# Performance work log

Measured on AMD Instinct MI355X. Metric: run time of the kernel, lower is better.

Reference implementation:

```python
import jax, jax.numpy as jnp
import numpy as np

EPS = 1e-5  # torch LayerNorm default eps
ALIBI_SLOPE = 1.0

def layer_norm(x, g, b):
    mu = x.mean(-1, keepdims=True)
    var = ((x - mu) ** 2).mean(-1, keepdims=True)
    return (x - mu) * jax.lax.rsqrt(var + EPS) * g + b

def setup_inputs() -> dict:
    key = jax.random.key(0)
    B, T, D, DK, F = 4, 4096, 1024, 128, 2048  # F = ffn_mult * d_model
    ks = jax.random.split(key, 6)
    def s(k, shp, fan):
        return jax.random.normal(k, shp, jnp.float32) / np.sqrt(fan).astype(np.float32)
    return {
        'x': jax.random.normal(ks[0], (B, T, D), jnp.float32),
        'ln1_g': jnp.ones((D,), jnp.float32), 'ln1_b': jnp.zeros((D,), jnp.float32),
        'Wq': s(ks[1], (DK, D), D),  # torch Linear weight layout (out, in)
        'Wk': s(ks[2], (DK, D), D),
        'Wv': s(ks[3], (D, D), D),
        'ln2_g': jnp.ones((D,), jnp.float32), 'ln2_b': jnp.zeros((D,), jnp.float32),
        'W1': s(ks[4], (F, D), D), 'b1': jnp.zeros((F,), jnp.float32),
        'W2': s(ks[5], (D, F), F), 'b2': jnp.zeros((D,), jnp.float32),
    }

def reference(x, ln1_g, ln1_b, Wq, Wk, Wv, ln2_g, ln2_b, W1, b1, W2, b2):
    B, T, D = x.shape
    dk = Wq.shape[0]
    h = layer_norm(x, ln1_g, ln1_b)
    q = jnp.einsum('btd,kd->btk', h, Wq)
    k = jnp.einsum('btd,kd->btk', h, Wk)
    att = jnp.einsum('btk,bsk->bts', q, k) * (dk ** -0.5)  # [B,T,T]
    pos = jnp.arange(T)
    dist = jnp.clip(pos[:, None] - pos[None, :], 0).astype(att.dtype)
    att = att - ALIBI_SLOPE * dist  # alibi bias
    causal = pos[:, None] >= pos[None, :]
    att = jnp.where(causal, att, -jnp.inf)
    att = jax.nn.softmax(att, axis=-1)
    ctx = jnp.einsum('bts,bsd->btd', att, h)  # note: attends over h, not a v-projection
    x = x + jnp.einsum('btd,ed->bte', ctx, Wv)
    h2 = layer_norm(x, ln2_g, ln2_b)
    ff = jnp.maximum(jnp.einsum('btd,fd->btf', h2, W1) + b1, 0.0)
    x = x + jnp.einsum('btf,df->btd', ff, W2) + b2
    return x
```

## Files before the change

kernel.cpp:

```cpp
#include <hip/hip_runtime.h>
#include <stdint.h>

typedef __attribute__((ext_vector_type(4))) float f32x4;
typedef __attribute__((ext_vector_type(8))) unsigned short u16x8;
typedef __attribute__((ext_vector_type(4))) unsigned short u16x4;
typedef unsigned short bf16_t;

#define DEV __device__ __forceinline__

DEV void mfma16(f32x4& d, u16x8 a, u16x8 b) {
    asm("v_mfma_f32_16x16x32_bf16 %0, %1, %2, %0" : "+v"(d) : "v"(a), "v"(b));
}

DEV bf16_t f2bf(float f) {
    uint32_t u = __builtin_bit_cast(uint32_t, f);
    return (bf16_t)((u + 0x7fffu + ((u >> 16) & 1u)) >> 16);
}

DEV void async_g2l16(const void* g, void* l) {
    __builtin_amdgcn_global_load_lds(
        (const __attribute__((address_space(1))) uint32_t*)(uintptr_t)g,
        (__attribute__((address_space(3))) uint32_t*)(uint32_t)(uintptr_t)l,
        16, 0, 0);
}

DEV void blockbar() {
    asm volatile("" ::: "memory");
    __builtin_amdgcn_s_barrier();
    asm volatile("" ::: "memory");
}

#define VMCNT(n) asm volatile("s_waitcnt vmcnt(" #n ")" ::: "memory")

#define MFMA_QUAD(M0, AF, BF)                                                                              \
    __builtin_amdgcn_s_setprio(1);                                                                         \
    mfma16(acc[M0+0][0],AF[0],BF[0]); mfma16(acc[M0+0][1],AF[0],BF[1]); mfma16(acc[M0+0][2],AF[0],BF[2]); mfma16(acc[M0+0][3],AF[0],BF[3]); \
    mfma16(acc[M0+1][0],AF[1],BF[0]); mfma16(acc[M0+1][1],AF[1],BF[1]); mfma16(acc[M0+1][2],AF[1],BF[2]); mfma16(acc[M0+1][3],AF[1],BF[3]); \
    mfma16(acc[M0+2][0],AF[2],BF[0]); mfma16(acc[M0+2][1],AF[2],BF[1]); mfma16(acc[M0+2][2],AF[2],BF[2]); mfma16(acc[M0+2][3],AF[2],BF[3]); \
    mfma16(acc[M0+3][0],AF[3],BF[0]); mfma16(acc[M0+3][1],AF[3],BF[1]); mfma16(acc[M0+3][2],AF[3],BF[2]); mfma16(acc[M0+3][3],AF[3],BF[3]); \
    __builtin_amdgcn_s_setprio(0)

template <int EPI>
__global__ __launch_bounds__(512, 2) void gemm256_nt(
    const bf16_t* __restrict__ A, const bf16_t* __restrict__ B,
    void* __restrict__ Cp, const float* __restrict__ bias,
    const float* __restrict__ res, int M, int N, int K)
{
    __shared__ bf16_t sA[4 * 8192];
    __shared__ bf16_t sB[4 * 8192];
    const int tid = threadIdx.x;
    const int wave = tid >> 6, lane = tid & 63;
    const int lcol = lane & 15, krow = lane >> 4;
    const int wm = wave >> 2, wn = wave & 3;

    int id  = blockIdx.y * gridDim.x + blockIdx.x;
    int nwg = gridDim.x * gridDim.y;
    int swz = ((nwg & 7) == 0) ? ((id & 7) * (nwg >> 3) + (id >> 3)) : id;
    const int bn = swz % gridDim.y;
    const int bm = swz / gridDim.y;
    const int row_a = bm * 256, col_c = bn * 256;

    const int tq = tid >> 2;
    const int tr = (((tid & 3) ^ ((tid >> 3) & 3)) * 8);
    const bf16_t* aSt = A + (size_t)(row_a + tq) * K + tr;
    const bf16_t* bSt = B + (size_t)(col_c + tq) * K + tr;
    const size_t rowstep = (size_t)128 * K;
    bf16_t* ldsAw = sA + wave * 512;
    bf16_t* ldsBw = sB + wave * 512;

    const int cswz = (krow ^ ((lcol >> 1) & 3)) * 8;
    const int raOff = (wm * 128 + lcol) * 32 + cswz;
    const int rbOff = (wn * 64  + lcol) * 32 + cswz;

    f32x4 acc[8][4] = {};
    const int nt = K >> 6;

    async_g2l16(aSt,                ldsAw);
    async_g2l16(aSt + rowstep,      ldsAw + 4096);
    async_g2l16(bSt,                ldsBw);
    async_g2l16(bSt + rowstep,      ldsBw + 4096);
    async_g2l16(aSt + 32,           ldsAw + 8192);
    async_g2l16(aSt + 32 + rowstep, ldsAw + 8192 + 4096);
    async_g2l16(bSt + 32,           ldsBw + 8192);
    async_g2l16(bSt + 32 + rowstep, ldsBw + 8192 + 4096);
    VMCNT(4);
    blockbar();

    for (int t = 0; t < nt; ++t) {
        const int rbase = (t & 1) ? 16384 : 0;
        const int wbase = (t & 1) ? 0 : 16384;
        const bool pf = (t + 1) < nt;
        const size_t ko = (size_t)(t + 1) * 64;
        u16x8 fa[4], fb[4];

#pragma unroll
        for (int i = 0; i < 4; i++) fa[i] = *(const u16x8*)&sA[rbase + raOff + i * 512];
#pragma unroll
        for (int i = 0; i < 4; i++) fb[i] = *(const u16x8*)&sB[rbase + rbOff + i * 512];
        if (pf) { async_g2l16(aSt + ko,           ldsAw + wbase);
                  async_g2l16(aSt + ko + rowstep, ldsAw + wbase + 4096); }
        blockbar();
        MFMA_QUAD(0, fa, fb);
        blockbar();

#pragma unroll
        for (int i = 0; i < 4; i++) fa[i] = *(const u16x8*)&sA[rbase + raOff + 2048 + i * 512];
        if (pf) { async_g2l16(bSt + ko,           ldsBw + wbase);
                  async_g2l16(bSt + ko + rowstep, ldsBw + wbase + 4096); }
        blockbar();
        MFMA_QUAD(4, fa, fb);
        if (pf) { VMCNT(4); } else { VMCNT(0); }
        blockbar();

#pragma unroll
        for (int i = 0; i < 4; i++) fa[i] = *(const u16x8*)&sA[rbase + 8192 + raOff + i * 512];
#pragma unroll
        for (int i = 0; i < 4; i++) fb[i] = *(const u16x8*)&sB[rbase + 8192 + rbOff + i * 512];
        if (pf) { async_g2l16(aSt + ko + 32,           ldsAw + wbase + 8192);
                  async_g2l16(aSt + ko + 32 + rowstep, ldsAw + wbase + 8192 + 4096); }
        blockbar();
        MFMA_QUAD(0, fa, fb);
        blockbar();

#pragma unroll
        for (int i = 0; i < 4; i++) fa[i] = *(const u16x8*)&sA[rbase + 8192 + raOff + 2048 + i * 512];
        if (pf) { async_g2l16(bSt + ko + 32,           ldsBw + wbase + 8192);
                  async_g2l16(bSt + ko + 32 + rowstep, ldsBw + wbase + 8192 + 4096); }
        blockbar();
        MFMA_QUAD(4, fa, fb);
        if (pf) { VMCNT(4); }
        blockbar();
    }

#pragma unroll
    for (int mi = 0; mi < 8; mi++)
#pragma unroll
        for (int ni = 0; ni < 4; ni++)
#pragma unroll
            for (int j = 0; j < 4; j++) {
                const int gr = row_a + wm * 128 + mi * 16 + krow * 4 + j;
                const int gc = col_c + wn * 64 + ni * 16 + lcol;
                float v = acc[mi][ni][j];
                if (EPI == 0) {
                    ((bf16_t*)Cp)[(size_t)gr * N + gc] = f2bf(v);
                } else if (EPI == 1) {
                    v += bias[gc];
                    v = fmaxf(v, 0.f);
                    ((bf16_t*)Cp)[(size_t)gr * N + gc] = f2bf(v);
                } else if (EPI == 2) {
                    ((float*)Cp)[(size_t)gr * N + gc] = v + res[(size_t)gr * N + gc];
                } else {
                    ((float*)Cp)[(size_t)gr * N + gc] = v + bias[gc] + res[(size_t)gr * N + gc];
                }
            }
}

template <int EPI>
__global__ __launch_bounds__(256) void gemm_nt(
    const bf16_t* __restrict__ A, const bf16_t* __restrict__ B,
    void* __restrict__ Cp, const float* __restrict__ bias,
    const float* __restrict__ res, int M, int N, int K)
{
    alignas(16) __shared__ bf16_t sA[128 * 32];
    alignas(16) __shared__ bf16_t sB[128 * 32];
    const int tid = threadIdx.x;
    const int wave = tid >> 6, lane = tid & 63;
    const int lcol = lane & 15, krow = lane >> 4;

    int id  = blockIdx.y * gridDim.x + blockIdx.x;
    int nwg = gridDim.x * gridDim.y;
    int swz = ((nwg & 7) == 0) ? ((id & 7) * (nwg >> 3) + (id >> 3)) : id;
    const int bn = swz % gridDim.y;
    const int bm = swz / gridDim.y;

    const int row_a = bm * 128, col_c = bn * 128;
    const int wm = (wave >> 1) * 64, wn = (wave & 1) * 64;

    const int   srow  = wave * 16 + (lane >> 2);
    const int   scol  = (lane & 3) * 8;
    const bf16_t* aSrc = A + (size_t)(row_a + srow) * K + scol;
    const bf16_t* bSrc = B + (size_t)(col_c + srow) * K + scol;
    char* sAl = (char*)sA + wave * 1024;
    char* sBl = (char*)sB + wave * 1024;
    const size_t rstep = (size_t)64 * K;

    f32x4 acc[4][4] = {};

    for (int k0 = 0; k0 < K; k0 += 32) {
        async_g2l16(aSrc + k0,         sAl);
        async_g2l16(aSrc + k0 + rstep, sAl + 4096);
        async_g2l16(bSrc + k0,         sBl);
        async_g2l16(bSrc + k0 + rstep, sBl + 4096);
        __syncthreads();
        u16x8 af[4], bfr[4];
#pragma unroll
        for (int i = 0; i < 4; i++) {
            af[i]  = *(const u16x8*)&sA[(wm + i * 16 + lcol) * 32 + krow * 8];
            bfr[i] = *(const u16x8*)&sB[(wn + i * 16 + lcol) * 32 + krow * 8];
        }
#pragma unroll
        for (int mi = 0; mi < 4; mi++)
#pragma unroll
            for (int ni = 0; ni < 4; ni++)
                mfma16(acc[mi][ni], af[mi], bfr[ni]);
        __syncthreads();
    }

#pragma unroll
    for (int mi = 0; mi < 4; mi++)
#pragma unroll
        for (int ni = 0; ni < 4; ni++)
#pragma unroll
            for (int j = 0; j < 4; j++) {
                const int gr = row_a + wm + mi * 16 + krow * 4 + j;
                const int gc = col_c + wn + ni * 16 + lcol;
                float v = acc[mi][ni][j];
                if (EPI == 0) {
                    ((bf16_t*)Cp)[(size_t)gr * N + gc] = f2bf(v);
                } else if (EPI == 1) {
                    v += bias[gc];
                    v = fmaxf(v, 0.f);
                    ((bf16_t*)Cp)[(size_t)gr * N + gc] = f2bf(v);
                } else if (EPI == 2) {
                    ((float*)Cp)[(size_t)gr * N + gc] = v + res[(size_t)gr * N + gc];
                } else {
                    ((float*)Cp)[(size_t)gr * N + gc] = v + bias[gc] + res[(size_t)gr * N + gc];
                }
            }
}

__global__ __launch_bounds__(256) void ln_kernel(
    const float* __restrict__ X, const float* __restrict__ G,
    const float* __restrict__ Bt, bf16_t* __restrict__ O)
{
    const int row = blockIdx.x, tid = threadIdx.x;
    const int wave = tid >> 6, lane = tid & 63;
    const size_t base = (size_t)row * 1024 + tid * 4;
    f32x4 xv = *(const f32x4*)&X[base];
    float s  = xv[0] + xv[1] + xv[2] + xv[3];
    float s2 = xv[0]*xv[0] + xv[1]*xv[1] + xv[2]*xv[2] + xv[3]*xv[3];
#pragma unroll
    for (int o = 1; o < 64; o <<= 1) { s += __shfl_xor(s, o); s2 += __shfl_xor(s2, o); }
    __shared__ float red[8];
    if (lane == 0) { red[wave] = s; red[wave + 4] = s2; }
    __syncthreads();
    s  = red[0] + red[1] + red[2] + red[3];
    s2 = red[4] + red[5] + red[6] + red[7];
    const float mu = s * (1.f / 1024.f);
    const float rs = rsqrtf(s2 * (1.f / 1024.f) - mu * mu + 1e-5f);
    f32x4 gv = *(const f32x4*)&G[tid * 4];
    f32x4 bv = *(const f32x4*)&Bt[tid * 4];
    u16x4 ov;
#pragma unroll
    for (int i = 0; i < 4; i++) ov[i] = f2bf((xv[i] - mu) * rs * gv[i] + bv[i]);
    *(u16x4*)&O[base] = ov;
}

__global__ __launch_bounds__(256) void cvt_f32_bf16(
    const float* __restrict__ src, bf16_t* __restrict__ dst, int n)
{
    int i = (blockIdx.x * 256 + threadIdx.x) * 4;
    if (i >= n) return;
    f32x4 v = *(const f32x4*)&src[i];
    u16x4 o;
#pragma unroll
    for (int t = 0; t < 4; t++) o[t] = f2bf(v[t]);
    *(u16x4*)&dst[i] = o;
}

__global__ __launch_bounds__(256) void attn_p(
    const bf16_t* __restrict__ QK, bf16_t* __restrict__ P, int T)
{
    const int tid = threadIdx.x, w = tid >> 6, lane = tid & 63;
    const int lcol = lane & 15, krow = lane >> 4;
    const int qt = blockIdx.x;
    const int ntb = T >> 6;
    const int b = qt / ntb;
    const int r0 = (qt - b * ntb) << 6;
    const size_t g0 = (size_t)b * T + r0;
    const int jbase = r0 - 192;
    const float scale = 0.08838834764831845f;

    __shared__ float lred[2][4][64];

    u16x8 qf[4][4];
#pragma unroll
    for (int mf = 0; mf < 4; mf++)
#pragma unroll
        for (int ks = 0; ks < 4; ks++)
            qf[mf][ks] = *(const u16x8*)&QK[(g0 + mf * 16 + lcol) * 256 + ks * 32 + krow * 8];

    f32x4 acc[4][4] = {};
    const size_t kbase = (size_t)b * T * 256 + 128;
#pragma unroll
    for (int ks = 0; ks < 4; ks++) {
        u16x8 kf[4];
#pragma unroll
        for (int nf = 0; nf < 4; nf++) {
            int jc = jbase + w * 64 + nf * 16 + lcol;
            int jr = jc < 0 ? 0 : jc;
            kf[nf] = *(const u16x8*)&QK[kbase + (size_t)jr * 256 + ks * 32 + krow * 8];
        }
#pragma unroll
        for (int mf = 0; mf < 4; mf++)
#pragma unroll
            for (int nf = 0; nf < 4; nf++)
                mfma16(acc[mf][nf], qf[mf][ks], kf[nf]);
    }

#pragma unroll
    for (int mf = 0; mf < 4; mf++)
#pragma unroll
        for (int j = 0; j < 4; j++) {
            const int i_ = r0 + mf * 16 + krow * 4 + j;
            float m = -1e30f;
#pragma unroll
            for (int nf = 0; nf < 4; nf++) {
                const int jc = jbase + w * 64 + nf * 16 + lcol;
                float sv = (jc >= 0 && jc <= i_) ? acc[mf][nf][j] * scale - (float)(i_ - jc) : -1e30f;
                acc[mf][nf][j] = sv;
                m = fmaxf(m, sv);
            }
#pragma unroll
            for (int o = 1; o < 16; o <<= 1) m = fmaxf(m, __shfl_xor(m, o));
            if (lcol == 0) lred[0][w][mf * 16 + krow * 4 + j] = m;
        }
    __syncthreads();

#pragma unroll
    for (int mf = 0; mf < 4; mf++)
#pragma unroll
        for (int j = 0; j < 4; j++) {
            const int rr = mf * 16 + krow * 4 + j;
            const float m = fmaxf(fmaxf(lred[0][0][rr], lred[0][1][rr]),
                                  fmaxf(lred[0][2][rr], lred[0][3][rr]));
            float sm = 0.f;
#pragma unroll
            for (int nf = 0; nf < 4; nf++) {
                float p = __expf(acc[mf][nf][j] - m);
                acc[mf][nf][j] = p;
                sm += p;
            }
#pragma unroll
            for (int o = 1; o < 16; o <<= 1) sm += __shfl_xor(sm, o);
            if (lcol == 0) lred[1][w][rr] = sm;
        }
    __syncthreads();

    float inv_l[4][4];
#pragma unroll
    for (int mf = 0; mf < 4; mf++)
#pragma unroll
        for (int j = 0; j < 4; j++) {
            const int rr = mf * 16 + krow * 4 + j;
            inv_l[mf][j] = 1.f / (lred[1][0][rr] + lred[1][1][rr] + lred[1][2][rr] + lred[1][3][rr]);
        }
#pragma unroll
    for (int mf = 0; mf < 4; mf++)
#pragma unroll
        for (int nf = 0; nf < 4; nf++)
#pragma unroll
            for (int j = 0; j < 4; j++) {
                const int rr = mf * 16 + krow * 4 + j;
                P[((size_t)qt * 64 + rr) * 256 + w * 64 + nf * 16 + lcol] =
                    f2bf(acc[mf][nf][j] * inv_l[mf][j]);
            }
}

__global__ __launch_bounds__(256) void pv_gemm(
    const bf16_t* __restrict__ P, const bf16_t* __restrict__ H,
    bf16_t* __restrict__ CTX, int T)
{
    alignas(16) __shared__ bf16_t sHt[128 * 40];
    const int tid = threadIdx.x, w = tid >> 6, lane = tid & 63;
    const int lcol = lane & 15, krow = lane >> 4;
    const int qt = blockIdx.x, d0 = blockIdx.y * 128;
    const int ntb = T >> 6, b = qt / ntb;
    const int r0 = (qt - b * ntb) << 6;
    const int jbase = r0 - 192;
    const int wm = (w >> 1) * 32, wn = (w & 1) * 64;
    const int kk = tid >> 3, seg = tid & 7;

    f32x4 acc[2][4] = {};
    for (int k0 = 0; k0 < 256; k0 += 32) {
        int j = jbase + k0 + kk;
        if (j < 0) j = 0;
        const bf16_t* hp = H + ((size_t)b * T + j) * 1024 + d0 + seg * 16;
        u16x8 v0 = *(const u16x8*)hp;
        u16x8 v1 = *(const u16x8*)(hp + 8);
        __syncthreads();
#pragma unroll
        for (int i = 0; i < 8; i++) {
            sHt[(seg * 16 + i) * 40 + kk]     = v0[i];
            sHt[(seg * 16 + 8 + i) * 40 + kk] = v1[i];
        }
        __syncthreads();
        u16x8 af[2], bfr[4];
#pragma unroll
        for (int mi = 0; mi < 2; mi++)
            af[mi] = *(const u16x8*)&P[((size_t)qt * 64 + wm + mi * 16 + lcol) * 256 + k0 + krow * 8];
#pragma unroll
        for (int ni = 0; ni < 4; ni++)
            bfr[ni] = *(const u16x8*)&sHt[(wn + ni * 16 + lcol) * 40 + krow * 8];
#pragma unroll
        for (int mi = 0; mi < 2; mi++)
#pragma unroll
            for (int ni = 0; ni < 4; ni++)
                mfma16(acc[mi][ni], af[mi], bfr[ni]);
    }
#pragma unroll
    for (int mi = 0; mi < 2; mi++)
#pragma unroll
        for (int ni = 0; ni < 4; ni++)
#pragma unroll
            for (int j = 0; j < 4; j++)
                CTX[((size_t)b * T + r0 + wm + mi * 16 + krow * 4 + j) * 1024 +
                    d0 + wn + ni * 16 + lcol] = f2bf(acc[mi][ni][j]);
}

extern "C" void kernel_launch(void* const* d_in, const int* in_sizes, int n_in,
                              void* d_out, int out_size, void* d_ws, size_t ws_size,
                              hipStream_t stream)
{
    const float* x   = (const float*)d_in[0];
    const float* g1  = (const float*)d_in[1];
    const float* be1 = (const float*)d_in[2];
    const float* Wq  = (const float*)d_in[3];
    const float* Wk  = (const float*)d_in[4];
    const float* Wv  = (const float*)d_in[5];
    const float* g2  = (const float*)d_in[6];
    const float* be2 = (const float*)d_in[7];
    const float* W1  = (const float*)d_in[8];
    const float* b1  = (const float*)d_in[9];
    const float* W2  = (const float*)d_in[10];
    const float* b2  = (const float*)d_in[11];

    const int B = 4, T = 4096, D = 1024, DK = 128, F = 2048;
    const int BT = B * T;

    char* ws = (char*)d_ws;
    size_t off = 0;
    auto alloc = [&](size_t bytes) {
        void* p = ws + off;
        off += (bytes + 255) & ~(size_t)255;
        return p;
    };
    bf16_t* wqk_b = (bf16_t*)alloc((size_t)2 * DK * D * 2);
    bf16_t* wv_b  = (bf16_t*)alloc((size_t)D * D * 2);
    bf16_t* w1_b  = (bf16_t*)alloc((size_t)F * D * 2);
    bf16_t* w2_b  = (bf16_t*)alloc((size_t)D * F * 2);
    bf16_t* h     = (bf16_t*)alloc((size_t)BT * D * 2);
    bf16_t* qk    = (bf16_t*)alloc((size_t)BT * 256 * 2);
    bf16_t* P     = (bf16_t*)alloc((size_t)BT * 256 * 2);
    bf16_t* ctx   = (bf16_t*)alloc((size_t)BT * D * 2);
    bf16_t* ff    = (bf16_t*)alloc((size_t)BT * F * 2);
    if (ws_size < off) return;
    float* x2 = (float*)d_out;

    cvt_f32_bf16<<<DK * D / 1024, 256, 0, stream>>>(Wq, wqk_b, DK * D);
    cvt_f32_bf16<<<DK * D / 1024, 256, 0, stream>>>(Wk, wqk_b + (size_t)DK * D, DK * D);
    cvt_f32_bf16<<<D * D / 1024, 256, 0, stream>>>(Wv, wv_b, D * D);
    cvt_f32_bf16<<<F * D / 1024, 256, 0, stream>>>(W1, w1_b, F * D);
    cvt_f32_bf16<<<D * F / 1024, 256, 0, stream>>>(W2, w2_b, D * F);

    ln_kernel<<<BT, 256, 0, stream>>>(x, g1, be1, h);

    gemm_nt<0><<<dim3(BT / 128, 2), 256, 0, stream>>>(h, wqk_b, qk, nullptr, nullptr, BT, 256, D);

    attn_p<<<BT / 64, 256, 0, stream>>>(qk, P, T);
    pv_gemm<<<dim3(BT / 64, D / 128), 256, 0, stream>>>(P, h, ctx, T);

    gemm256_nt<2><<<dim3(BT / 256, D / 256), 512, 0, stream>>>(ctx, wv_b, x2, nullptr, x, BT, D, D);

    ln_kernel<<<BT, 256, 0, stream>>>(x2, g2, be2, h);

    gemm256_nt<1><<<dim3(BT / 256, F / 256), 512, 0, stream>>>(h, w1_b, ff, b1, nullptr, BT, F, D);

    gemm256_nt<3><<<dim3(BT / 256, D / 256), 512, 0, stream>>>(ff, w2_b, x2, b2, x2, BT, D, F);
}
```

Measured before the change: 346.7 us.

## Shrink GEMM tile to 256x128 with K-step 32 and simpler double buffer

Replaces the 256x256 GEMM with a 256x128 tile that uses a 32-wide K step, a single-stage double buffer and one barrier per iteration. It also raises the occupancy hint from 2 to 4 blocks. Halving LDS and accumulator registers per block is meant to give more resident blocks and more tiles across the CUs for these mid-sized GEMMs. In exchange, each loaded byte is reused less, the wait and barrier run every 32 K, and the finer interleave of loads and MFMAs is lost.

Result: slower. 360.4 us (+4.0%).

```diff
diff --git a/kernel.cpp b/kernel.cpp
--- a/kernel.cpp
+++ b/kernel.cpp
@@ -32,33 +32,25 @@
 
 #define VMCNT(n) asm volatile("s_waitcnt vmcnt(" #n ")" ::: "memory")
 
-#define MFMA_QUAD(M0, AF, BF)                                                                              \
-    __builtin_amdgcn_s_setprio(1);                                                                         \
-    mfma16(acc[M0+0][0],AF[0],BF[0]); mfma16(acc[M0+0][1],AF[0],BF[1]); mfma16(acc[M0+0][2],AF[0],BF[2]); mfma16(acc[M0+0][3],AF[0],BF[3]); \
-    mfma16(acc[M0+1][0],AF[1],BF[0]); mfma16(acc[M0+1][1],AF[1],BF[1]); mfma16(acc[M0+1][2],AF[1],BF[2]); mfma16(acc[M0+1][3],AF[1],BF[3]); \
-    mfma16(acc[M0+2][0],AF[2],BF[0]); mfma16(acc[M0+2][1],AF[2],BF[1]); mfma16(acc[M0+2][2],AF[2],BF[2]); mfma16(acc[M0+2][3],AF[2],BF[3]); \
-    mfma16(acc[M0+3][0],AF[3],BF[0]); mfma16(acc[M0+3][1],AF[3],BF[1]); mfma16(acc[M0+3][2],AF[3],BF[2]); mfma16(acc[M0+3][3],AF[3],BF[3]); \
-    __builtin_amdgcn_s_setprio(0)
-
 template <int EPI>
-__global__ __launch_bounds__(512, 2) void gemm256_nt(
+__global__ __launch_bounds__(512, 4) void gemm256x128_nt(
     const bf16_t* __restrict__ A, const bf16_t* __restrict__ B,
     void* __restrict__ Cp, const float* __restrict__ bias,
     const float* __restrict__ res, int M, int N, int K)
 {
-    __shared__ bf16_t sA[4 * 8192];
-    __shared__ bf16_t sB[4 * 8192];
+    __shared__ bf16_t sA[2 * 8192];
+    __shared__ bf16_t sB[2 * 4096];
     const int tid = threadIdx.x;
     const int wave = tid >> 6, lane = tid & 63;
     const int lcol = lane & 15, krow = lane >> 4;
-    const int wm = wave >> 2, wn = wave & 3;
+    const int wm = wave >> 1, wn = wave & 1;
 
     int id  = blockIdx.y * gridDim.x + blockIdx.x;
     int nwg = gridDim.x * gridDim.y;
     int swz = ((nwg & 7) == 0) ? ((id & 7) * (nwg >> 3) + (id >> 3)) : id;
     const int bn = swz % gridDim.y;
     const int bm = swz / gridDim.y;
-    const int row_a = bm * 256, col_c = bn * 256;
+    const int row_a = bm * 256, col_c = bn * 128;
 
     const int tq = tid >> 2;
     const int tr = (((tid & 3) ^ ((tid >> 3) & 3)) * 8);
@@ -69,76 +61,52 @@
     bf16_t* ldsBw = sB + wave * 512;
 
     const int cswz = (krow ^ ((lcol >> 1) & 3)) * 8;
-    const int raOff = (wm * 128 + lcol) * 32 + cswz;
-    const int rbOff = (wn * 64  + lcol) * 32 + cswz;
-
-    f32x4 acc[8][4] = {};
-    const int nt = K >> 6;
-
-    async_g2l16(aSt,                ldsAw);
-    async_g2l16(aSt + rowstep,      ldsAw + 4096);
-    async_g2l16(bSt,                ldsBw);
-    async_g2l16(bSt + rowstep,      ldsBw + 4096);
-    async_g2l16(aSt + 32,           ldsAw + 8192);
-    async_g2l16(aSt + 32 + rowstep, ldsAw + 8192 + 4096);
-    async_g2l16(bSt + 32,           ldsBw + 8192);
-    async_g2l16(bSt + 32 + rowstep, ldsBw + 8192 + 4096);
-    VMCNT(4);
+    const int raOff = (wm * 64 + lcol) * 32 + cswz;
+    const int rbOff = (wn * 64 + lcol) * 32 + cswz;
+
+    f32x4 acc[4][4] = {};
+    const int nt = K >> 5;
+
+    async_g2l16(aSt,           ldsAw);
+    async_g2l16(aSt + rowstep, ldsAw + 4096);
+    async_g2l16(bSt,           ldsBw);
+    VMCNT(0);
     blockbar();
 
     for (int t = 0; t < nt; ++t) {
-        const int rbase = (t & 1) ? 16384 : 0;
-        const int wbase = (t & 1) ? 0 : 16384;
+        const int ra = (t & 1) ? 8192 : 0;
+        const int rb = (t & 1) ? 4096 : 0;
+        const int wa = 8192 - ra, wb = 4096 - rb;
         const bool pf = (t + 1) < nt;
-        const size_t ko = (size_t)(t + 1) * 64;
+        const size_t ko = (size_t)(t + 1) * 32;
         u16x8 fa[4], fb[4];
-
-#pragma unroll
-        for (int i = 0; i < 4; i++) fa[i] = *(const u16x8*)&sA[rbase + raOff + i * 512];
-#pragma unroll
-        for (int i = 0; i < 4; i++) fb[i] = *(const u16x8*)&sB[rbase + rbOff + i * 512];
-        if (pf) { async_g2l16(aSt + ko,           ldsAw + wbase);
-                  async_g2l16(aSt + ko + rowstep, ldsAw + wbase + 4096); }
-        blockbar();
-        MFMA_QUAD(0, fa, fb);
-        blockbar();
-
-#pragma unroll
-        for (int i = 0; i < 4; i++) fa[i] = *(const u16x8*)&sA[rbase + raOff + 2048 + i * 512];
-        if (pf) { async_g2l16(bSt + ko,           ldsBw + wbase);
-                  async_g2l16(bSt + ko + rowstep, ldsBw + wbase + 4096); }
-        blockbar();
-        MFMA_QUAD(4, fa, fb);
-        if (pf) { VMCNT(4); } else { VMCNT(0); }
-        blockbar();
-
-#pragma unroll
-        for (int i = 0; i < 4; i++) fa[i] = *(const u16x8*)&sA[rbase + 8192 + raOff + i * 512];
-#pragma unroll
-        for (int i = 0; i < 4; i++) fb[i] = *(const u16x8*)&sB[rbase + 8192 + rbOff + i * 512];
-        if (pf) { async_g2l16(aSt + ko + 32,           ldsAw + wbase + 8192);
-                  async_g2l16(aSt + ko + 32 + rowstep, ldsAw + wbase + 8192 + 4096); }
-        blockbar();
-        MFMA_QUAD(0, fa, fb);
-        blockbar();
-
-#pragma unroll
-        for (int i = 0; i < 4; i++) fa[i] = *(const u16x8*)&sA[rbase + 8192 + raOff + 2048 + i * 512];
-        if (pf) { async_g2l16(bSt + ko + 32,           ldsBw + wbase + 8192);
-                  async_g2l16(bSt + ko + 32 + rowstep, ldsBw + wbase + 8192 + 4096); }
-        blockbar();
-        MFMA_QUAD(4, fa, fb);
-        if (pf) { VMCNT(4); }
+#pragma unroll
+        for (int i = 0; i < 4; i++) fa[i] = *(const u16x8*)&sA[ra + raOff + i * 512];
+#pragma unroll
+        for (int i = 0; i < 4; i++) fb[i] = *(const u16x8*)&sB[rb + rbOff + i * 512];
+        if (pf) {
+            async_g2l16(aSt + ko,           ldsAw + wa);
+            async_g2l16(aSt + ko + rowstep, ldsAw + wa + 4096);
+            async_g2l16(bSt + ko,           ldsBw + wb);
+        }
+        __builtin_amdgcn_s_setprio(1);
+#pragma unroll
+        for (int mi = 0; mi < 4; mi++)
+#pragma unroll
+            for (int ni = 0; ni < 4; ni++)
+                mfma16(acc[mi][ni], fa[mi], fb[ni]);
+        __builtin_amdgcn_s_setprio(0);
+        VMCNT(0);
         blockbar();
     }
 
 #pragma unroll
-    for (int mi = 0; mi < 8; mi++)
+    for (int mi = 0; mi < 4; mi++)
 #pragma unroll
         for (int ni = 0; ni < 4; ni++)
 #pragma unroll
             for (int j = 0; j < 4; j++) {
-                const int gr = row_a + wm * 128 + mi * 16 + krow * 4 + j;
+                const int gr = row_a + wm * 64 + mi * 16 + krow * 4 + j;
                 const int gc = col_c + wn * 64 + ni * 16 + lcol;
                 float v = acc[mi][ni][j];
                 if (EPI == 0) {
@@ -470,11 +438,11 @@
     attn_p<<<BT / 64, 256, 0, stream>>>(qk, P, T);
     pv_gemm<<<dim3(BT / 64, D / 128), 256, 0, stream>>>(P, h, ctx, T);
 
-    gemm256_nt<2><<<dim3(BT / 256, D / 256), 512, 0, stream>>>(ctx, wv_b, x2, nullptr, x, BT, D, D);
+    gemm256x128_nt<2><<<dim3(BT / 256, D / 128), 512, 0, stream>>>(ctx, wv_b, x2, nullptr, x, BT, D, D);
 
     ln_kernel<<<BT, 256, 0, stream>>>(x2, g2, be2, h);
 
-    gemm256_nt<1><<<dim3(BT / 256, F / 256), 512, 0, stream>>>(h, w1_b, ff, b1, nullptr, BT, F, D);
-
-    gemm256_nt<3><<<dim3(BT / 256, D / 256), 512, 0, stream>>>(ff, w2_b, x2, b2, x2, BT, D, F);
-}
+    gemm256x128_nt<1><<<dim3(BT / 256, F / 128), 512, 0, stream>>>(h, w1_b, ff, b1, nullptr, BT, F, D);
+
+    gemm256x128_nt<3><<<dim3(BT / 256, D / 128), 512, 0, stream>>>(ff, w2_b, x2, b2, x2, BT, D, F);
+}
```

## Software-pipeline LDS fragment loads with MFMA using double register fragments

Applied to the files above, without the earlier changes.

Restructures the GEMM main loop so each stage issues its LDS fragment reads for the next quad while the current MFMA quad runs, using separate A/B register fragment sets. Fragments for the next K tile are prefetched at the end of each iteration, and the barriers per iteration drop from eight to four with tighter vmcnt waits. The goal is to hide LDS latency and cut synchronisation stalls. The cost is more registers, which could reduce occupancy, and a more delicate ordering of async loads against barriers, with some risk of races.

Result: faster. 336.5 us (-2.9%).

```diff
diff --git a/kernel.cpp b/kernel.cpp
--- a/kernel.cpp
+++ b/kernel.cpp
@@ -72,6 +72,7 @@
     const int raOff = (wm * 128 + lcol) * 32 + cswz;
     const int rbOff = (wn * 64  + lcol) * 32 + cswz;
 
+    u16x8 faA[4], faB[4], fbA[4], fbB[4];
     f32x4 acc[8][4] = {};
     const int nt = K >> 6;
 
@@ -86,49 +87,51 @@
     VMCNT(4);
     blockbar();
 
+#pragma unroll
+    for (int i = 0; i < 4; i++) faA[i] = *(const u16x8*)&sA[raOff + i * 512];
+#pragma unroll
+    for (int i = 0; i < 4; i++) fbA[i] = *(const u16x8*)&sB[rbOff + i * 512];
+
     for (int t = 0; t < nt; ++t) {
         const int rbase = (t & 1) ? 16384 : 0;
-        const int wbase = (t & 1) ? 0 : 16384;
+        const int wbase = 16384 - rbase;
         const bool pf = (t + 1) < nt;
         const size_t ko = (size_t)(t + 1) * 64;
-        u16x8 fa[4], fb[4];
-
-#pragma unroll
-        for (int i = 0; i < 4; i++) fa[i] = *(const u16x8*)&sA[rbase + raOff + i * 512];
-#pragma unroll
-        for (int i = 0; i < 4; i++) fb[i] = *(const u16x8*)&sB[rbase + rbOff + i * 512];
+
+#pragma unroll
+        for (int i = 0; i < 4; i++) faB[i] = *(const u16x8*)&sA[rbase + raOff + 2048 + i * 512];
         if (pf) { async_g2l16(aSt + ko,           ldsAw + wbase);
                   async_g2l16(aSt + ko + rowstep, ldsAw + wbase + 4096); }
+        MFMA_QUAD(0, faA, fbA);
+        VMCNT(2);
         blockbar();
-        MFMA_QUAD(0, fa, fb);
-        blockbar();
-
-#pragma unroll
-        for (int i = 0; i < 4; i++) fa[i] = *(const u16x8*)&sA[rbase + raOff + 2048 + i * 512];
+
+#pragma unroll
+        for (int i = 0; i < 4; i++) faA[i] = *(const u16x8*)&sA[rbase + 8192 + raOff + i * 512];
+#pragma unroll
+        for (int i = 0; i < 4; i++) fbB[i] = *(const u16x8*)&sB[rbase + 8192 + rbOff + i * 512];
         if (pf) { async_g2l16(bSt + ko,           ldsBw + wbase);
                   async_g2l16(bSt + ko + rowstep, ldsBw + wbase + 4096); }
+        MFMA_QUAD(4, faB, fbA);
         blockbar();
-        MFMA_QUAD(4, fa, fb);
-        if (pf) { VMCNT(4); } else { VMCNT(0); }
-        blockbar();
-
-#pragma unroll
-        for (int i = 0; i < 4; i++) fa[i] = *(const u16x8*)&sA[rbase + 8192 + raOff + i * 512];
-#pragma unroll
-        for (int i = 0; i < 4; i++) fb[i] = *(const u16x8*)&sB[rbase + 8192 + rbOff + i * 512];
+
+#pragma unroll
+        for (int i = 0; i < 4; i++) faB[i] = *(const u16x8*)&sA[rbase + 8192 + raOff + 2048 + i * 512];
         if (pf) { async_g2l16(aSt + ko + 32,           ldsAw + wbase + 8192);
                   async_g2l16(aSt + ko + 32 + rowstep, ldsAw + wbase + 8192 + 4096); }
+        MFMA_QUAD(0, faA, fbB);
+        VMCNT(2);
         blockbar();
-        MFMA_QUAD(0, fa, fb);
-        blockbar();
-
-#pragma unroll
-        for (int i = 0; i < 4; i++) fa[i] = *(const u16x8*)&sA[rbase + 8192 + raOff + 2048 + i * 512];
-        if (pf) { async_g2l16(bSt + ko + 32,           ldsBw + wbase + 8192);
-                  async_g2l16(bSt + ko + 32 + rowstep, ldsBw + wbase + 8192 + 4096); }
-        blockbar();
-        MFMA_QUAD(4, fa, fb);
-        if (pf) { VMCNT(4); }
+
+        if (pf) {
+#pragma unroll
+            for (int i = 0; i < 4; i++) faA[i] = *(const u16x8*)&sA[wbase + raOff + i * 512];
+#pragma unroll
+            for (int i = 0; i < 4; i++) fbA[i] = *(const u16x8*)&sB[wbase + rbOff + i * 512];
+            async_g2l16(bSt + ko + 32,           ldsBw + wbase + 8192);
+            async_g2l16(bSt + ko + 32 + rowstep, ldsBw + wbase + 8192 + 4096);
+        }
+        MFMA_QUAD(4, faB, fbB);
         blockbar();
     }
 
```
